# Performance work log

Measured on AMD Instinct MI355X. Metric: run time of the kernel, lower is better.

The kernel has to match this reference:

```python
import jax, jax.numpy as jnp
import numpy as np

B, T, CM, CZ, H = 2, 512, 256, 128, 16
DH = CM // H  # 16
EPS = 1e-5


def setup_inputs() -> dict:
    root = jax.random.key(0)
    ks = jax.random.split(root, 16)
    n = lambda i, shape: jax.random.normal(ks[i], shape, dtype=jnp.float32)
    s = np.float32(1.0 / np.sqrt(CM))
    return dict(
        query=n(0, (B, T, CM)),
        key=n(1, (B, T, CM)),
        value=n(2, (B, T, CM)),
        pos_embedding=n(3, (B, 2 * T - 1, CM)),  # T2 = 2T-1 relative positions
        z=n(4, (B, T, T, CZ)),
        mask=jax.random.randint(ks[5], (B, 1, T), 0, 2) > 0,
        Wq=n(6, (CM, CM)) * s, bq=jnp.zeros((CM,), jnp.float32),
        Wk=n(7, (CM, CM)) * s, bk=jnp.zeros((CM,), jnp.float32),
        Wv=n(8, (CM, CM)) * s, bv=jnp.zeros((CM,), jnp.float32),
        Wp=n(9, (CM, CM)) * s,
        u_bias=n(10, (H, DH)) * np.float32(0.1),
        v_bias=n(11, (H, DH)) * np.float32(0.1),
        Wo=n(12, (CM, CM)) * s, bo=jnp.zeros((CM,), jnp.float32),
        ln_g=jnp.ones((CZ,), jnp.float32), ln_b=jnp.zeros((CZ,), jnp.float32),
        Wz=n(13, (CZ, H)) * np.float32(1.0 / np.sqrt(CZ)),
    )


def _relative_shift(ps):
    # ps: (B, H, T1, T2) -> Transformer-XL relative shift, keep first T2//2+1 cols
    b, h, t1, t2 = ps.shape
    padded = jnp.pad(ps, ((0, 0), (0, 0), (0, 0), (1, 0)))  # (b,h,t1,t2+1)
    padded = padded.reshape(b, h, t2 + 1, t1)
    shifted = padded[:, :, 1:, :].reshape(b, h, t1, t2)
    return shifted[..., : t2 // 2 + 1]


def reference(query, key, value, pos_embedding, z, mask,
              Wq, bq, Wk, bk, Wv, bv, Wp, u_bias, v_bias, Wo, bo,
              ln_g, ln_b, Wz):
    b = query.shape[0]
    q = (query @ Wq.T + bq).reshape(b, -1, H, DH)          # (b,T,H,dh)
    k = (key @ Wk.T + bk).reshape(b, -1, H, DH)
    v = (value @ Wv.T + bv).reshape(b, -1, H, DH)
    p = (pos_embedding @ Wp.T).reshape(b, -1, H, DH)       # (b,2T-1,H,dh)

    content = jnp.einsum('bihd,bjhd->bhij', q + u_bias, k)     # (b,H,T,T)
    pos = jnp.einsum('bihd,bjhd->bhij', q + v_bias, p)         # (b,H,T,2T-1)
    pos = _relative_shift(pos)                                  # (b,H,T,T)

    # z bias: LayerNorm over c_z then project to heads (chunking in torch is a no-op math-wise)
    mu = jnp.mean(z, axis=-1, keepdims=True)
    var = jnp.var(z, axis=-1, keepdims=True)
    zn = (z - mu) * jax.lax.rsqrt(var + EPS) * ln_g + ln_b
    z_bias = jnp.einsum('bijc,ch->bhij', zn, Wz)                # (b,H,T,T)

    score = (content + pos) / np.float32(np.sqrt(DH)) + z_bias
    score = jnp.where(mask[:, None, :, :], jnp.float32(-10000.0), score)
    attn = jax.nn.softmax(score, axis=-1)  # dropout is identity in eval

    ctx = jnp.einsum('bhij,bjhd->bihd', attn, v).reshape(b, -1, CM)
    return ctx @ Wo.T + bo
```

## Files before the change

### kernel.cpp

```cpp
#include <hip/hip_runtime.h>
#include <hip/hip_bf16.h>

typedef __attribute__((ext_vector_type(8))) short short8;
typedef __attribute__((ext_vector_type(4))) short short4v;
typedef __attribute__((ext_vector_type(4))) float f32x4;

#define LD4(dst, v4) { dst[0]=(v4).x; dst[1]=(v4).y; dst[2]=(v4).z; dst[3]=(v4).w; }

static __device__ __forceinline__ short f2bf(float f) {
    union { float f; unsigned u; } v; v.f = f;
    unsigned r = (v.u + 0x7FFFu + ((v.u >> 16) & 1u)) >> 16;
    return (short)r;
}
static __device__ __forceinline__ float bf2f(short s) {
    union { unsigned u; float f; } v; v.u = ((unsigned)(unsigned short)s) << 16;
    return v.f;
}

static __device__ __forceinline__ void proj_tile(
    const float* __restrict__ X, const float* __restrict__ W,
    const float* __restrict__ bias, float* __restrict__ Yf,
    short* __restrict__ Yb, int M, int base, float* xs)
{
    int rt = base >> 1, ct = base & 1;
    int t = threadIdx.x;
    int row_base = rt * 32;
    {
        int r = t >> 3, k0 = (t & 7) * 32;
        int row = row_base + r;
        if (row < M) {
            const float* xp = X + (size_t)row * 256 + k0;
            #pragma unroll
            for (int q = 0; q < 8; ++q) {
                float4 v = *(const float4*)(xp + q * 4);
                xs[(k0 + q * 4 + 0) * 36 + r] = v.x;
                xs[(k0 + q * 4 + 1) * 36 + r] = v.y;
                xs[(k0 + q * 4 + 2) * 36 + r] = v.z;
                xs[(k0 + q * 4 + 3) * 36 + r] = v.w;
            }
        } else {
            #pragma unroll
            for (int q = 0; q < 32; ++q) xs[(k0 + q) * 36 + r] = 0.f;
        }
    }
    __syncthreads();
    int c_base = ct * 128 + (t & 31) * 4;
    int r_base = (t >> 5) * 4;
    float acc[4][4];
    #pragma unroll
    for (int a = 0; a < 4; ++a)
        #pragma unroll
        for (int b = 0; b < 4; ++b) acc[a][b] = 0.f;
    for (int k = 0; k < 256; k += 4) {
        float w0[4], w1[4], w2[4], w3[4];
        { float4 v = *(const float4*)(W + (size_t)(c_base + 0) * 256 + k); LD4(w0, v); }
        { float4 v = *(const float4*)(W + (size_t)(c_base + 1) * 256 + k); LD4(w1, v); }
        { float4 v = *(const float4*)(W + (size_t)(c_base + 2) * 256 + k); LD4(w2, v); }
        { float4 v = *(const float4*)(W + (size_t)(c_base + 3) * 256 + k); LD4(w3, v); }
        #pragma unroll
        for (int kk = 0; kk < 4; ++kk) {
            float xl[4];
            float4 xv = *(const float4*)(&xs[(k + kk) * 36 + r_base]);
            LD4(xl, xv);
            #pragma unroll
            for (int ri = 0; ri < 4; ++ri) {
                acc[ri][0] += xl[ri] * w0[kk];
                acc[ri][1] += xl[ri] * w1[kk];
                acc[ri][2] += xl[ri] * w2[kk];
                acc[ri][3] += xl[ri] * w3[kk];
            }
        }
    }
    #pragma unroll
    for (int ri = 0; ri < 4; ++ri) {
        int row = row_base + r_base + ri;
        if (row < M) {
            float o0 = acc[ri][0] + (bias ? bias[c_base + 0] : 0.f);
            float o1 = acc[ri][1] + (bias ? bias[c_base + 1] : 0.f);
            float o2 = acc[ri][2] + (bias ? bias[c_base + 2] : 0.f);
            float o3 = acc[ri][3] + (bias ? bias[c_base + 3] : 0.f);
            if (Yb) {
                short4v o; o[0] = f2bf(o0); o[1] = f2bf(o1); o[2] = f2bf(o2); o[3] = f2bf(o3);
                *(short4v*)(Yb + (size_t)row * 256 + c_base) = o;
            } else {
                float4 o; o.x = o0; o.y = o1; o.z = o2; o.w = o3;
                *(float4*)(Yf + (size_t)row * 256 + c_base) = o;
            }
        }
    }
}

__global__ void k_proj(const float* __restrict__ query, const float* __restrict__ key,
                       const float* __restrict__ value, const float* __restrict__ pos,
                       const float* __restrict__ Wq, const float* __restrict__ bq,
                       const float* __restrict__ Wk, const float* __restrict__ bk,
                       const float* __restrict__ Wv, const float* __restrict__ bv,
                       const float* __restrict__ Wp,
                       const float* __restrict__ ln_g, const float* __restrict__ ln_b,
                       const float* __restrict__ Wz, const int* __restrict__ mask,
                       float* __restrict__ qb, short* __restrict__ kbf,
                       short* __restrict__ vbf, short* __restrict__ pbf,
                       short* __restrict__ wzp, float* __restrict__ Ch,
                       int* __restrict__ idx, int* __restrict__ cnt)
{
    __shared__ float xs[256 * 36];
    int bx = blockIdx.x;
    if (bx == 320) {
        int lane = threadIdx.x & 63, wave = threadIdx.x >> 6;
        if (wave == 0) {
            for (int b = 0; b < 2; ++b) {
                int* idxb = idx + b * 512;
                #pragma unroll
                for (int q = 0; q < 8; ++q) idxb[q * 64 + lane] = -1;
                int total = 0;
                for (int q = 0; q < 8; ++q) {
                    int j = q * 64 + lane;
                    int u = (mask[b * 512 + j] == 0) ? 1 : 0;
                    unsigned long long bal = __ballot(u);
                    int p = total + __popcll(bal & ((1ull << lane) - 1ull));
                    if (u) idxb[p] = j;
                    total += (int)__popcll(bal);
                }
                if (total == 0) {
                    for (int q = 0; q < 8; ++q) idxb[q * 64 + lane] = q * 64 + lane;
                    total = 512;
                }
                if (lane == 0) cnt[b] = total;
            }
        } else if (wave == 1) {
            for (int id = lane; id < 2048; id += 64) {
                int m = id >> 9, rem = id & 511, l = rem >> 3, ii = rem & 7;
                int c = m * 32 + ((l >> 4) << 3) + ii, h = l & 15;
                wzp[id] = f2bf(ln_g[c] * Wz[c * 16 + h]);
            }
        } else if (wave == 2) {
            if (lane < 16) {
                float cc = 0.f;
                for (int c = 0; c < 128; ++c) cc += ln_b[c] * Wz[c * 16 + lane];
                Ch[lane] = cc;
            }
        }
        return;
    }
    if (bx < 64)       proj_tile(query, Wq, bq, qb, nullptr, 1024, bx, xs);
    else if (bx < 128) proj_tile(key,   Wk, bk, nullptr, kbf, 1024, bx - 64, xs);
    else if (bx < 192) proj_tile(value, Wv, bv, nullptr, vbf, 1024, bx - 128, xs);
    else               proj_tile(pos,   Wp, nullptr, nullptr, pbf, 2046, bx - 192, xs);
}

__global__ void __launch_bounds__(256, 6) k_zc(
    const float* __restrict__ z, const short* __restrict__ wzp,
    const int* __restrict__ idx, const int* __restrict__ cnt,
    const short* __restrict__ kbf, const short* __restrict__ vbf,
    short* __restrict__ kbfC, short* __restrict__ vbTC,
    short* __restrict__ zacc, float* __restrict__ rsbuf)
{
    __shared__ short st[32 * 264];
    int bx = blockIdx.x;
    const short8 z8 = {0,0,0,0,0,0,0,0};
    if (bx < 32) {
        int b = bx >> 4, jn0 = (bx & 15) * 32;
        int t = threadIdx.x;
        int r = t >> 3, cc = (t & 7) * 32;
        int jn = jn0 + r;
        int jv = idx[b * 512 + jn];
        {
            short* dst = kbfC + ((size_t)b * 512 + jn) * 256 + cc;
            if (jv >= 0) {
                const short* src = kbf + ((size_t)b * 512 + jv) * 256 + cc;
                #pragma unroll
                for (int q = 0; q < 4; ++q) *(short8*)(dst + q * 8) = *(const short8*)(src + q * 8);
            } else {
                #pragma unroll
                for (int q = 0; q < 4; ++q) *(short8*)(dst + q * 8) = z8;
            }
        }
        {
            if (jv >= 0) {
                const short* src = vbf + ((size_t)b * 512 + jv) * 256 + cc;
                #pragma unroll
                for (int q = 0; q < 4; ++q) *(short8*)(&st[r * 264 + cc + q * 8]) = *(const short8*)(src + q * 8);
            } else {
                #pragma unroll
                for (int q = 0; q < 4; ++q) *(short8*)(&st[r * 264 + cc + q * 8]) = z8;
            }
            __syncthreads();
            int c = t;
            short tmp[32];
            #pragma unroll
            for (int q = 0; q < 32; ++q) tmp[q] = st[q * 264 + c];
            short* dst = vbTC + ((size_t)b * 256 + c) * 512 + jn0;
            #pragma unroll
            for (int q = 0; q < 4; ++q) *(short8*)(dst + q * 8) = *(const short8*)(&tmp[q * 8]);
        }
        return;
    }
    int wave = threadIdx.x >> 6, lane = threadIdx.x & 63;
    int w = (bx - 32) * 4 + wave;
    int bi = w >> 5, tl = w & 31;
    int b = bi >> 9;
    int np = (min(cnt[b], 512) + 31) & ~31;
    if (tl * 16 >= np) return;
    int h = lane & 15, g = lane >> 4;
    short8 wz[4];
    #pragma unroll
    for (int m = 0; m < 4; ++m) wz[m] = *(const short8*)(wzp + m * 512 + lane * 8);
    int jv = idx[b * 512 + tl * 16 + h];
    int jr = (jv < 0) ? 0 : jv;
    const float* zr = z + ((size_t)bi * 512 + jr) * 128 + g * 8;
    float4 xa[4], xb[4];
    #pragma unroll
    for (int m = 0; m < 4; ++m) {
        xa[m] = *(const float4*)(zr + m * 32);
        xb[m] = *(const float4*)(zr + m * 32 + 4);
    }
    float sum = 0.f, sq = 0.f;
    #pragma unroll
    for (int m = 0; m < 4; ++m) {
        sum += xa[m].x + xa[m].y + xa[m].z + xa[m].w + xb[m].x + xb[m].y + xb[m].z + xb[m].w;
        sq  += xa[m].x*xa[m].x + xa[m].y*xa[m].y + xa[m].z*xa[m].z + xa[m].w*xa[m].w
             + xb[m].x*xb[m].x + xb[m].y*xb[m].y + xb[m].z*xb[m].z + xb[m].w*xb[m].w;
    }
    sum += __shfl_xor(sum, 16); sum += __shfl_xor(sum, 32);
    sq  += __shfl_xor(sq, 16);  sq  += __shfl_xor(sq, 32);
    float mu = sum * (1.f / 128.f);
    float rs = rsqrtf(sq * (1.f / 128.f) - mu * mu + 1e-5f);
    f32x4 acc = {0.f, 0.f, 0.f, 0.f};
    #pragma unroll
    for (int m = 0; m < 4; ++m) {
        short8 af;
        af[0] = f2bf(xa[m].x - mu); af[1] = f2bf(xa[m].y - mu);
        af[2] = f2bf(xa[m].z - mu); af[3] = f2bf(xa[m].w - mu);
        af[4] = f2bf(xb[m].x - mu); af[5] = f2bf(xb[m].y - mu);
        af[6] = f2bf(xb[m].z - mu); af[7] = f2bf(xb[m].w - mu);
        acc = __builtin_amdgcn_mfma_f32_16x16x32_bf16(af, wz[m], acc, 0, 0, 0);
    }
    short4v o; o[0] = f2bf(acc[0]); o[1] = f2bf(acc[1]); o[2] = f2bf(acc[2]); o[3] = f2bf(acc[3]);
    *(short4v*)(zacc + ((size_t)bi * 16 + h) * 512 + tl * 16 + g * 4) = o;
    if (g == 0) rsbuf[(size_t)bi * 512 + tl * 16 + h] = rs;
}

__global__ void __launch_bounds__(256, 4) k_attn3(
    const float* __restrict__ qb, const short* __restrict__ kbfC, const short* __restrict__ pbf,
    const short* __restrict__ zacc, const float* __restrict__ rsbuf, const float* __restrict__ Ch,
    const float* __restrict__ u_bias, const float* __restrict__ v_bias,
    const int* __restrict__ idx, const int* __restrict__ cnt,
    const short* __restrict__ vbTC, float* __restrict__ ctx)
{
    __shared__ short wT[16 * 520];
    __shared__ float redm[64], reds[64];
    const short8 zero8 = {0, 0, 0, 0, 0, 0, 0, 0};

    int bi = blockIdx.x;
    int b = bi >> 9, i = bi & 511;
    int t = threadIdx.x;
    int lane = t & 63, wave = t >> 6;
    int h = lane & 15, g = lane >> 4;
    float ch = Ch[h];
    int np = (min(cnt[b], 512) + 31) & ~31;
    int nt16 = np >> 4;

    bool act = ((h & 1) == (g >> 1));
    int m_act = act ? (h >> 1) : 8;
    short8 qu8 = zero8, qv8 = zero8;
    {
        int c0q = h * 16 + (g & 1) * 8;
        const float* qp = qb + (size_t)bi * 256 + c0q;
        #pragma unroll
        for (int ii = 0; ii < 8; ++ii) {
            float qv_ = qp[ii];
            qu8[ii] = f2bf(0.25f * (qv_ + u_bias[c0q + ii]));
            qv8[ii] = f2bf(0.25f * (qv_ + v_bias[c0q + ii]));
        }
        if (!act) { qu8 = zero8; qv8 = zero8; }
    }

    f32x4 sc[8];
    float mloc = -3.0e38f;
    #pragma unroll
    for (int q = 0; q < 8; ++q) {
        int tl = wave + q * 4;
        if (tl < nt16) {
            int jn = tl * 16 + h;
            int jvh = idx[b * 512 + jn];
            int jrp = 511 + ((jvh < 0) ? 0 : jvh) - i;
            const short* kr = kbfC + ((size_t)b * 512 + jn) * 256 + g * 8;
            const short* pr = pbf + ((size_t)b * 1023 + jrp) * 256 + g * 8;
            f32x4 acp = {0.f, 0.f, 0.f, 0.f};
            #pragma unroll
            for (int m = 0; m < 8; ++m) {
                short8 ka = *(const short8*)(kr + m * 32);
                short8 pa = *(const short8*)(pr + m * 32);
                short8 bu = (m == m_act) ? qu8 : zero8;
                short8 bv = (m == m_act) ? qv8 : zero8;
                acp = __builtin_amdgcn_mfma_f32_16x16x32_bf16(ka, bu, acp, 0, 0, 0);
                acp = __builtin_amdgcn_mfma_f32_16x16x32_bf16(pa, bv, acp, 0, 0, 0);
            }
            short4v za = *(const short4v*)(zacc + ((size_t)bi * 16 + h) * 512 + tl * 16 + g * 4);
            float4 rs4 = *(const float4*)(rsbuf + (size_t)bi * 512 + tl * 16 + g * 4);
            int4 jv4 = *(const int4*)(idx + b * 512 + tl * 16 + g * 4);
            float rr[4]; LD4(rr, rs4);
            int jj4[4]; jj4[0] = jv4.x; jj4[1] = jv4.y; jj4[2] = jv4.z; jj4[3] = jv4.w;
            #pragma unroll
            for (int reg = 0; reg < 4; ++reg) {
                float s = acp[reg] + rr[reg] * bf2f(za[reg]) + ch;
                s = (jj4[reg] < 0) ? -3.0e38f : s;
                sc[q][reg] = s;
                mloc = fmaxf(mloc, s);
            }
        }
    }

    mloc = fmaxf(mloc, __shfl_xor(mloc, 16));
    mloc = fmaxf(mloc, __shfl_xor(mloc, 32));
    redm[wave * 16 + h] = mloc;
    __syncthreads();
    float mg = fmaxf(fmaxf(redm[h], redm[16 + h]), fmaxf(redm[32 + h], redm[48 + h]));
    float ssum = 0.f;
    #pragma unroll
    for (int q = 0; q < 8; ++q) {
        int tl = wave + q * 4;
        if (tl < nt16) {
            #pragma unroll
            for (int reg = 0; reg < 4; ++reg) {
                float e = __expf(sc[q][reg] - mg);
                sc[q][reg] = e;
                ssum += e;
            }
        }
    }
    ssum += __shfl_xor(ssum, 16); ssum += __shfl_xor(ssum, 32);
    reds[wave * 16 + h] = ssum;
    __syncthreads();
    float sg = reds[h] + reds[16 + h] + reds[32 + h] + reds[48 + h];
    float inv = 1.f / sg;
    #pragma unroll
    for (int q = 0; q < 8; ++q) {
        int tl = wave + q * 4;
        if (tl < nt16) {
            short4v w4;
            #pragma unroll
            for (int reg = 0; reg < 4; ++reg) w4[reg] = f2bf(sc[q][reg] * inv);
            *(short4v*)(&wT[h * 520 + tl * 16 + g * 4]) = w4;
        }
    }
    __syncthreads();

    #pragma unroll
    for (int q = 0; q < 4; ++q) {
        int hp = wave * 4 + q;
        int c0 = hp * 16;
        const short* vrow = vbTC + ((size_t)b * 256 + c0 + h) * 512;
        f32x4 a0 = {0.f, 0.f, 0.f, 0.f};
        for (int jn0 = 0; jn0 < np; jn0 += 32) {
            short8 wA = *(const short8*)(&wT[hp * 520 + jn0 + g * 8]);
            short8 vB = *(const short8*)(vrow + jn0 + g * 8);
            a0 = __builtin_amdgcn_mfma_f32_16x16x32_bf16(wA, vB, a0, 0, 0, 0);
        }
        if (g == 0) ctx[(size_t)bi * 256 + c0 + h] = a0[0];
    }
}

__global__ void proj_o(const float* __restrict__ X, const float* __restrict__ W,
                       const float* __restrict__ bias, float* __restrict__ Y)
{
    __shared__ float xs[256 * 36];
    proj_tile(X, W, bias, Y, nullptr, 1024, blockIdx.x, xs);
}

extern "C" void kernel_launch(void* const* d_in, const int* in_sizes, int n_in,
                              void* d_out, int out_size, void* d_ws, size_t ws_size,
                              hipStream_t stream) {
    const float* query = (const float*)d_in[0];
    const float* key   = (const float*)d_in[1];
    const float* value = (const float*)d_in[2];
    const float* pos   = (const float*)d_in[3];
    const float* z     = (const float*)d_in[4];
    const int*   mask  = (const int*)d_in[5];
    const float* Wq = (const float*)d_in[6];
    const float* bq = (const float*)d_in[7];
    const float* Wk = (const float*)d_in[8];
    const float* bk = (const float*)d_in[9];
    const float* Wv = (const float*)d_in[10];
    const float* bv = (const float*)d_in[11];
    const float* Wp = (const float*)d_in[12];
    const float* u_bias = (const float*)d_in[13];
    const float* v_bias = (const float*)d_in[14];
    const float* Wo = (const float*)d_in[15];
    const float* bo = (const float*)d_in[16];
    const float* ln_g = (const float*)d_in[17];
    const float* ln_b = (const float*)d_in[18];
    const float* Wz = (const float*)d_in[19];

    char* ws = (char*)d_ws;
    float* qb   = (float*)(ws + 0);
    short* kbf  = (short*)(ws + (1u << 20));
    short* vbf  = (short*)(ws + 1572864u);
    short* pbf  = (short*)(ws + (2u << 20));
    short* wzp  = (short*)(ws + (3u << 20));
    float* Ch   = (float*)(ws + (3u << 20) + 4096);
    int*   idx  = (int*)(ws + (3u << 20) + 8192);
    int*   cnt  = (int*)(ws + (3u << 20) + 16384);
    short* kbfC = (short*)(ws + (4u << 20));
    short* vbTC = (short*)(ws + 4718592u);
    short* zacc = (short*)(ws + (5u << 20));
    float* rsbuf= (float*)(ws + (22u << 20));
    float* ctx  = (float*)(ws + (24u << 20));

    hipLaunchKernelGGL(k_proj, dim3(321), dim3(256), 0, stream,
                       query, key, value, pos, Wq, bq, Wk, bk, Wv, bv, Wp,
                       ln_g, ln_b, Wz, mask,
                       qb, kbf, vbf, pbf, wzp, Ch, idx, cnt);
    hipLaunchKernelGGL(k_zc, dim3(8224), dim3(256), 0, stream,
                       z, wzp, idx, cnt, kbf, vbf, kbfC, vbTC, zacc, rsbuf);
    hipLaunchKernelGGL(k_attn3, dim3(1024), dim3(256), 0, stream,
                       qb, kbfC, pbf, zacc, rsbuf, Ch, u_bias, v_bias, idx, cnt, vbTC, ctx);
    hipLaunchKernelGGL(proj_o, dim3(64), dim3(256), 0, stream, ctx, Wo, bo, (float*)d_out);
}
```

Measured before the change: 191.2 us.

## Fold LayerNorm mean/scale into z-bias epilogue and halve projection tile rows

The z LayerNorm is refactored so raw z is converted to bf16 and fed to the MFMA directly. The mean and rstd are applied afterwards via a precomputed per-head sum of ln_g*Wz (Ah), and the final z-bias is finalised inside k_z. This removes the rsbuf buffer and its per-score load and FMA in the attention kernel, and shortens the z kernel's register lifetime. Projection tiles shrink from 32 to 16 rows, doubling block counts for k_proj and proj_o to improve occupancy on the many-CU GPU. The cost is more redundant W reads per block and some bf16 precision risk, since z is quantised before its mean is subtracted.

```diff
diff --git a/kernel.cpp b/kernel.cpp
--- a/kernel.cpp
+++ b/kernel.cpp
@@ -17,38 +17,38 @@
     return v.f;
 }
 
-static __device__ __forceinline__ void proj_tile(
+static __device__ __forceinline__ void proj_tile16(
     const float* __restrict__ X, const float* __restrict__ W,
     const float* __restrict__ bias, float* __restrict__ Yf,
     short* __restrict__ Yb, int M, int base, float* xs)
 {
     int rt = base >> 1, ct = base & 1;
     int t = threadIdx.x;
-    int row_base = rt * 32;
+    int row_base = rt * 16;
     {
-        int r = t >> 3, k0 = (t & 7) * 32;
+        int r = t & 15, kq = (t >> 4) * 16;
         int row = row_base + r;
         if (row < M) {
-            const float* xp = X + (size_t)row * 256 + k0;
-            #pragma unroll
-            for (int q = 0; q < 8; ++q) {
+            const float* xp = X + (size_t)row * 256 + kq;
+            #pragma unroll
+            for (int q = 0; q < 4; ++q) {
                 float4 v = *(const float4*)(xp + q * 4);
-                xs[(k0 + q * 4 + 0) * 36 + r] = v.x;
-                xs[(k0 + q * 4 + 1) * 36 + r] = v.y;
-                xs[(k0 + q * 4 + 2) * 36 + r] = v.z;
-                xs[(k0 + q * 4 + 3) * 36 + r] = v.w;
+                xs[(kq + q * 4 + 0) * 18 + r] = v.x;
+                xs[(kq + q * 4 + 1) * 18 + r] = v.y;
+                xs[(kq + q * 4 + 2) * 18 + r] = v.z;
+                xs[(kq + q * 4 + 3) * 18 + r] = v.w;
             }
         } else {
             #pragma unroll
-            for (int q = 0; q < 32; ++q) xs[(k0 + q) * 36 + r] = 0.f;
+            for (int q = 0; q < 16; ++q) xs[(kq + q) * 18 + r] = 0.f;
         }
     }
     __syncthreads();
     int c_base = ct * 128 + (t & 31) * 4;
-    int r_base = (t >> 5) * 4;
-    float acc[4][4];
-    #pragma unroll
-    for (int a = 0; a < 4; ++a)
+    int r_base = (t >> 5) * 2;
+    float acc[2][4];
+    #pragma unroll
+    for (int a = 0; a < 2; ++a)
         #pragma unroll
         for (int b = 0; b < 4; ++b) acc[a][b] = 0.f;
     for (int k = 0; k < 256; k += 4) {
@@ -59,20 +59,16 @@
         { float4 v = *(const float4*)(W + (size_t)(c_base + 3) * 256 + k); LD4(w3, v); }
         #pragma unroll
         for (int kk = 0; kk < 4; ++kk) {
-            float xl[4];
-            float4 xv = *(const float4*)(&xs[(k + kk) * 36 + r_base]);
-            LD4(xl, xv);
-            #pragma unroll
-            for (int ri = 0; ri < 4; ++ri) {
-                acc[ri][0] += xl[ri] * w0[kk];
-                acc[ri][1] += xl[ri] * w1[kk];
-                acc[ri][2] += xl[ri] * w2[kk];
-                acc[ri][3] += xl[ri] * w3[kk];
-            }
-        }
-    }
-    #pragma unroll
-    for (int ri = 0; ri < 4; ++ri) {
+            float x0 = xs[(k + kk) * 18 + r_base];
+            float x1 = xs[(k + kk) * 18 + r_base + 1];
+            acc[0][0] += x0 * w0[kk]; acc[0][1] += x0 * w1[kk];
+            acc[0][2] += x0 * w2[kk]; acc[0][3] += x0 * w3[kk];
+            acc[1][0] += x1 * w0[kk]; acc[1][1] += x1 * w1[kk];
+            acc[1][2] += x1 * w2[kk]; acc[1][3] += x1 * w3[kk];
+        }
+    }
+    #pragma unroll
+    for (int ri = 0; ri < 2; ++ri) {
         int row = row_base + r_base + ri;
         if (row < M) {
             float o0 = acc[ri][0] + (bias ? bias[c_base + 0] : 0.f);
@@ -90,22 +86,23 @@
     }
 }
 
-__global__ void k_proj(const float* __restrict__ query, const float* __restrict__ key,
-                       const float* __restrict__ value, const float* __restrict__ pos,
-                       const float* __restrict__ Wq, const float* __restrict__ bq,
-                       const float* __restrict__ Wk, const float* __restrict__ bk,
-                       const float* __restrict__ Wv, const float* __restrict__ bv,
-                       const float* __restrict__ Wp,
-                       const float* __restrict__ ln_g, const float* __restrict__ ln_b,
-                       const float* __restrict__ Wz, const int* __restrict__ mask,
-                       float* __restrict__ qb, short* __restrict__ kbf,
-                       short* __restrict__ vbf, short* __restrict__ pbf,
-                       short* __restrict__ wzp, float* __restrict__ Ch,
-                       int* __restrict__ idx, int* __restrict__ cnt)
+__global__ void __launch_bounds__(256, 4) k_proj(
+    const float* __restrict__ query, const float* __restrict__ key,
+    const float* __restrict__ value, const float* __restrict__ pos,
+    const float* __restrict__ Wq, const float* __restrict__ bq,
+    const float* __restrict__ Wk, const float* __restrict__ bk,
+    const float* __restrict__ Wv, const float* __restrict__ bv,
+    const float* __restrict__ Wp,
+    const float* __restrict__ ln_g, const float* __restrict__ ln_b,
+    const float* __restrict__ Wz, const int* __restrict__ mask,
+    float* __restrict__ qb, short* __restrict__ kbf,
+    short* __restrict__ vbf, short* __restrict__ pbf,
+    short* __restrict__ wzp, float* __restrict__ Ah, float* __restrict__ Ch,
+    int* __restrict__ idx, int* __restrict__ cnt)
 {
-    __shared__ float xs[256 * 36];
+    __shared__ float xs[256 * 18];
     int bx = blockIdx.x;
-    if (bx == 320) {
+    if (bx == 640) {
         int lane = threadIdx.x & 63, wave = threadIdx.x >> 6;
         if (wave == 0) {
             for (int b = 0; b < 2; ++b) {
@@ -134,26 +131,32 @@
                 wzp[id] = f2bf(ln_g[c] * Wz[c * 16 + h]);
             }
         } else if (wave == 2) {
-            if (lane < 16) {
-                float cc = 0.f;
-                for (int c = 0; c < 128; ++c) cc += ln_b[c] * Wz[c * 16 + lane];
-                Ch[lane] = cc;
-            }
+            int h = lane & 15, part = lane >> 4;
+            float a = 0.f, c = 0.f;
+            #pragma unroll 4
+            for (int cc = part * 32; cc < part * 32 + 32; ++cc) {
+                float wv = Wz[cc * 16 + h];
+                a += ln_g[cc] * wv;
+                c += ln_b[cc] * wv;
+            }
+            a += __shfl_xor(a, 16); a += __shfl_xor(a, 32);
+            c += __shfl_xor(c, 16); c += __shfl_xor(c, 32);
+            if (part == 0) { Ah[h] = a; Ch[h] = c; }
         }
         return;
     }
-    if (bx < 64)       proj_tile(query, Wq, bq, qb, nullptr, 1024, bx, xs);
-    else if (bx < 128) proj_tile(key,   Wk, bk, nullptr, kbf, 1024, bx - 64, xs);
-    else if (bx < 192) proj_tile(value, Wv, bv, nullptr, vbf, 1024, bx - 128, xs);
-    else               proj_tile(pos,   Wp, nullptr, nullptr, pbf, 2046, bx - 192, xs);
-}
-
-__global__ void __launch_bounds__(256, 6) k_zc(
+    if (bx < 128)      proj_tile16(query, Wq, bq, qb, nullptr, 1024, bx, xs);
+    else if (bx < 256) proj_tile16(key,   Wk, bk, nullptr, kbf, 1024, bx - 128, xs);
+    else if (bx < 384) proj_tile16(value, Wv, bv, nullptr, vbf, 1024, bx - 256, xs);
+    else               proj_tile16(pos,   Wp, nullptr, nullptr, pbf, 2046, bx - 384, xs);
+}
+
+__global__ void __launch_bounds__(256, 6) k_z(
     const float* __restrict__ z, const short* __restrict__ wzp,
+    const float* __restrict__ Ah, const float* __restrict__ Ch,
     const int* __restrict__ idx, const int* __restrict__ cnt,
     const short* __restrict__ kbf, const short* __restrict__ vbf,
-    short* __restrict__ kbfC, short* __restrict__ vbTC,
-    short* __restrict__ zacc, float* __restrict__ rsbuf)
+    short* __restrict__ kbfC, short* __restrict__ vbTC, short* __restrict__ zacc)
 {
     __shared__ short st[32 * 264];
     int bx = blockIdx.x;
@@ -208,18 +211,18 @@
     int jv = idx[b * 512 + tl * 16 + h];
     int jr = (jv < 0) ? 0 : jv;
     const float* zr = z + ((size_t)bi * 512 + jr) * 128 + g * 8;
-    float4 xa[4], xb[4];
+    float sum = 0.f, sq = 0.f;
+    short8 af[4];
     #pragma unroll
     for (int m = 0; m < 4; ++m) {
-        xa[m] = *(const float4*)(zr + m * 32);
-        xb[m] = *(const float4*)(zr + m * 32 + 4);
-    }
-    float sum = 0.f, sq = 0.f;
-    #pragma unroll
-    for (int m = 0; m < 4; ++m) {
-        sum += xa[m].x + xa[m].y + xa[m].z + xa[m].w + xb[m].x + xb[m].y + xb[m].z + xb[m].w;
-        sq  += xa[m].x*xa[m].x + xa[m].y*xa[m].y + xa[m].z*xa[m].z + xa[m].w*xa[m].w
-             + xb[m].x*xb[m].x + xb[m].y*xb[m].y + xb[m].z*xb[m].z + xb[m].w*xb[m].w;
+        float4 a = *(const float4*)(zr + m * 32);
+        float4 c = *(const float4*)(zr + m * 32 + 4);
+        sum += a.x + a.y + a.z + a.w + c.x + c.y + c.z + c.w;
+        sq  += a.x*a.x + a.y*a.y + a.z*a.z + a.w*a.w + c.x*c.x + c.y*c.y + c.z*c.z + c.w*c.w;
+        short8 s8;
+        s8[0] = f2bf(a.x); s8[1] = f2bf(a.y); s8[2] = f2bf(a.z); s8[3] = f2bf(a.w);
+        s8[4] = f2bf(c.x); s8[5] = f2bf(c.y); s8[6] = f2bf(c.z); s8[7] = f2bf(c.w);
+        af[m] = s8;
     }
     sum += __shfl_xor(sum, 16); sum += __shfl_xor(sum, 32);
     sq  += __shfl_xor(sq, 16);  sq  += __shfl_xor(sq, 32);
@@ -227,22 +230,23 @@
     float rs = rsqrtf(sq * (1.f / 128.f) - mu * mu + 1e-5f);
     f32x4 acc = {0.f, 0.f, 0.f, 0.f};
     #pragma unroll
-    for (int m = 0; m < 4; ++m) {
-        short8 af;
-        af[0] = f2bf(xa[m].x - mu); af[1] = f2bf(xa[m].y - mu);
-        af[2] = f2bf(xa[m].z - mu); af[3] = f2bf(xa[m].w - mu);
-        af[4] = f2bf(xb[m].x - mu); af[5] = f2bf(xb[m].y - mu);
-        af[6] = f2bf(xb[m].z - mu); af[7] = f2bf(xb[m].w - mu);
-        acc = __builtin_amdgcn_mfma_f32_16x16x32_bf16(af, wz[m], acc, 0, 0, 0);
-    }
-    short4v o; o[0] = f2bf(acc[0]); o[1] = f2bf(acc[1]); o[2] = f2bf(acc[2]); o[3] = f2bf(acc[3]);
+    for (int m = 0; m < 4; ++m)
+        acc = __builtin_amdgcn_mfma_f32_16x16x32_bf16(af[m], wz[m], acc, 0, 0, 0);
+    float ah = Ah[h], ch = Ch[h];
+    short4v o;
+    #pragma unroll
+    for (int reg = 0; reg < 4; ++reg) {
+        int orow = g * 4 + reg;
+        float mo = __shfl(mu, orow);
+        float ro = __shfl(rs, orow);
+        o[reg] = f2bf(ro * (acc[reg] - mo * ah) + ch);
+    }
     *(short4v*)(zacc + ((size_t)bi * 16 + h) * 512 + tl * 16 + g * 4) = o;
-    if (g == 0) rsbuf[(size_t)bi * 512 + tl * 16 + h] = rs;
 }
 
 __global__ void __launch_bounds__(256, 4) k_attn3(
     const float* __restrict__ qb, const short* __restrict__ kbfC, const short* __restrict__ pbf,
-    const short* __restrict__ zacc, const float* __restrict__ rsbuf, const float* __restrict__ Ch,
+    const short* __restrict__ zacc,
     const float* __restrict__ u_bias, const float* __restrict__ v_bias,
     const int* __restrict__ idx, const int* __restrict__ cnt,
     const short* __restrict__ vbTC, float* __restrict__ ctx)
@@ -256,7 +260,6 @@
     int t = threadIdx.x;
     int lane = t & 63, wave = t >> 6;
     int h = lane & 15, g = lane >> 4;
-    float ch = Ch[h];
     int np = (min(cnt[b], 512) + 31) & ~31;
     int nt16 = np >> 4;
 
@@ -297,13 +300,11 @@
                 acp = __builtin_amdgcn_mfma_f32_16x16x32_bf16(pa, bv, acp, 0, 0, 0);
             }
             short4v za = *(const short4v*)(zacc + ((size_t)bi * 16 + h) * 512 + tl * 16 + g * 4);
-            float4 rs4 = *(const float4*)(rsbuf + (size_t)bi * 512 + tl * 16 + g * 4);
             int4 jv4 = *(const int4*)(idx + b * 512 + tl * 16 + g * 4);
-            float rr[4]; LD4(rr, rs4);
             int jj4[4]; jj4[0] = jv4.x; jj4[1] = jv4.y; jj4[2] = jv4.z; jj4[3] = jv4.w;
             #pragma unroll
             for (int reg = 0; reg < 4; ++reg) {
-                float s = acp[reg] + rr[reg] * bf2f(za[reg]) + ch;
+                float s = acp[reg] + bf2f(za[reg]);
                 s = (jj4[reg] < 0) ? -3.0e38f : s;
                 sc[q][reg] = s;
                 mloc = fmaxf(mloc, s);
@@ -361,11 +362,12 @@
     }
 }
 
-__global__ void proj_o(const float* __restrict__ X, const float* __restrict__ W,
-                       const float* __restrict__ bias, float* __restrict__ Y)
+__global__ void __launch_bounds__(256, 4) proj_o(
+    const float* __restrict__ X, const float* __restrict__ W,
+    const float* __restrict__ bias, float* __restrict__ Y)
 {
-    __shared__ float xs[256 * 36];
-    proj_tile(X, W, bias, Y, nullptr, 1024, blockIdx.x, xs);
+    __shared__ float xs[256 * 18];
+    proj_tile16(X, W, bias, Y, nullptr, 1024, blockIdx.x, xs);
 }
 
 extern "C" void kernel_launch(void* const* d_in, const int* in_sizes, int n_in,
@@ -398,22 +400,22 @@
     short* vbf  = (short*)(ws + 1572864u);
     short* pbf  = (short*)(ws + (2u << 20));
     short* wzp  = (short*)(ws + (3u << 20));
-    float* Ch   = (float*)(ws + (3u << 20) + 4096);
+    float* Ah   = (float*)(ws + (3u << 20) + 4096);
+    float* Ch   = (float*)(ws + (3u << 20) + 4160);
     int*   idx  = (int*)(ws + (3u << 20) + 8192);
     int*   cnt  = (int*)(ws + (3u << 20) + 16384);
     short* kbfC = (short*)(ws + (4u << 20));
     short* vbTC = (short*)(ws + 4718592u);
     short* zacc = (short*)(ws + (5u << 20));
-    float* rsbuf= (float*)(ws + (22u << 20));
-    float* ctx  = (float*)(ws + (24u << 20));
-
-    hipLaunchKernelGGL(k_proj, dim3(321), dim3(256), 0, stream,
+    float* ctx  = (float*)(ws + (22u << 20));
+
+    hipLaunchKernelGGL(k_proj, dim3(641), dim3(256), 0, stream,
                        query, key, value, pos, Wq, bq, Wk, bk, Wv, bv, Wp,
                        ln_g, ln_b, Wz, mask,
-                       qb, kbf, vbf, pbf, wzp, Ch, idx, cnt);
-    hipLaunchKernelGGL(k_zc, dim3(8224), dim3(256), 0, stream,
-                       z, wzp, idx, cnt, kbf, vbf, kbfC, vbTC, zacc, rsbuf);
+                       qb, kbf, vbf, pbf, wzp, Ah, Ch, idx, cnt);
+    hipLaunchKernelGGL(k_z, dim3(8224), dim3(256), 0, stream,
+                       z, wzp, Ah, Ch, idx, cnt, kbf, vbf, kbfC, vbTC, zacc);
     hipLaunchKernelGGL(k_attn3, dim3(1024), dim3(256), 0, stream,
-                       qb, kbfC, pbf, zacc, rsbuf, Ch, u_bias, v_bias, idx, cnt, vbTC, ctx);
-    hipLaunchKernelGGL(proj_o, dim3(64), dim3(256), 0, stream, ctx, Wo, bo, (float*)d_out);
-}
+                       qb, kbfC, pbf, zacc, u_bias, v_bias, idx, cnt, vbTC, ctx);
+    hipLaunchKernelGGL(proj_o, dim3(128), dim3(256), 0, stream, ctx, Wo, bo, (float*)d_out);
+}
```

Result: slower. 214.5 us (+12.1%).

## Fold LayerNorm affine into z-bias, stage z via LDS, fuse output projection

Applied to the files above, without the earlier changes.

The z LayerNorm is now applied algebraically after the Wz projection (rs*(acc - mu*A_h) + C_h), so the finished z-bias is written once and the separate rsbuf array and its reads in attention are dropped. z rows are gathered through LDS with coalesced float4 loads and packed to bf16 using v_cvt_pk_bf16_f32. The output projection with Wo is fused into the tail of the attention kernel, which removes the ctx round trip and one launch. The cost is a per-block 256x256 GEMV that rereads Wo in every one of the 1024 blocks, lower z precision because statistics are now computed from bf16-rounded values, and a lower occupancy hint on k_z.

```diff
diff --git a/kernel.cpp b/kernel.cpp
--- a/kernel.cpp
+++ b/kernel.cpp
@@ -15,6 +15,11 @@
 static __device__ __forceinline__ float bf2f(short s) {
     union { unsigned u; float f; } v; v.u = ((unsigned)(unsigned short)s) << 16;
     return v.f;
+}
+static __device__ __forceinline__ unsigned cvt_pk_bf16(float lo, float hi) {
+    unsigned r;
+    asm volatile("v_cvt_pk_bf16_f32 %0, %1, %2" : "=v"(r) : "v"(lo), "v"(hi));
+    return r;
 }
 
 static __device__ __forceinline__ void proj_tile(
@@ -100,7 +105,7 @@
                        const float* __restrict__ Wz, const int* __restrict__ mask,
                        float* __restrict__ qb, short* __restrict__ kbf,
                        short* __restrict__ vbf, short* __restrict__ pbf,
-                       short* __restrict__ wzp, float* __restrict__ Ch,
+                       short* __restrict__ wzp, float* __restrict__ Ah, float* __restrict__ Ch,
                        int* __restrict__ idx, int* __restrict__ cnt)
 {
     __shared__ float xs[256 * 36];
@@ -134,11 +139,17 @@
                 wzp[id] = f2bf(ln_g[c] * Wz[c * 16 + h]);
             }
         } else if (wave == 2) {
-            if (lane < 16) {
-                float cc = 0.f;
-                for (int c = 0; c < 128; ++c) cc += ln_b[c] * Wz[c * 16 + lane];
-                Ch[lane] = cc;
-            }
+            int h = lane & 15, part = lane >> 4;
+            float a = 0.f, c = 0.f;
+            #pragma unroll 4
+            for (int cc = part * 32; cc < part * 32 + 32; ++cc) {
+                float wv = Wz[cc * 16 + h];
+                a += ln_g[cc] * wv;
+                c += ln_b[cc] * wv;
+            }
+            a += __shfl_xor(a, 16); a += __shfl_xor(a, 32);
+            c += __shfl_xor(c, 16); c += __shfl_xor(c, 32);
+            if (part == 0) { Ah[h] = a; Ch[h] = c; }
         }
         return;
     }
@@ -148,17 +159,18 @@
     else               proj_tile(pos,   Wp, nullptr, nullptr, pbf, 2046, bx - 192, xs);
 }
 
-__global__ void __launch_bounds__(256, 6) k_zc(
+__global__ void __launch_bounds__(256, 4) k_z(
     const float* __restrict__ z, const short* __restrict__ wzp,
+    const float* __restrict__ Ah, const float* __restrict__ Ch,
     const int* __restrict__ idx, const int* __restrict__ cnt,
     const short* __restrict__ kbf, const short* __restrict__ vbf,
-    short* __restrict__ kbfC, short* __restrict__ vbTC,
-    short* __restrict__ zacc, float* __restrict__ rsbuf)
+    short* __restrict__ kbfC, short* __restrict__ vbTC, short* __restrict__ zacc)
 {
-    __shared__ short st[32 * 264];
+    __shared__ short ldsb[8448];
     int bx = blockIdx.x;
-    const short8 z8 = {0,0,0,0,0,0,0,0};
+    const short8 z8v = {0,0,0,0,0,0,0,0};
     if (bx < 32) {
+        short* st = ldsb;
         int b = bx >> 4, jn0 = (bx & 15) * 32;
         int t = threadIdx.x;
         int r = t >> 3, cc = (t & 7) * 32;
@@ -172,7 +184,7 @@
                 for (int q = 0; q < 4; ++q) *(short8*)(dst + q * 8) = *(const short8*)(src + q * 8);
             } else {
                 #pragma unroll
-                for (int q = 0; q < 4; ++q) *(short8*)(dst + q * 8) = z8;
+                for (int q = 0; q < 4; ++q) *(short8*)(dst + q * 8) = z8v;
             }
         }
         {
@@ -182,7 +194,7 @@
                 for (int q = 0; q < 4; ++q) *(short8*)(&st[r * 264 + cc + q * 8]) = *(const short8*)(src + q * 8);
             } else {
                 #pragma unroll
-                for (int q = 0; q < 4; ++q) *(short8*)(&st[r * 264 + cc + q * 8]) = z8;
+                for (int q = 0; q < 4; ++q) *(short8*)(&st[r * 264 + cc + q * 8]) = z8v;
             }
             __syncthreads();
             int c = t;
@@ -201,25 +213,42 @@
     int b = bi >> 9;
     int np = (min(cnt[b], 512) + 31) & ~31;
     if (tl * 16 >= np) return;
+    short* zs = ldsb + wave * 2112;
+    const int* idxr = idx + b * 512 + tl * 16;
+    const float* zb_ = z + (size_t)bi * 65536;
+    int l5 = lane >> 5, l31 = lane & 31;
+    int idxv = idxr[lane & 15];
+    #pragma unroll
+    for (int m = 0; m < 8; ++m) {
+        int r = 2 * m + l5;
+        int jv = __shfl(idxv, r);
+        int jr = (jv < 0) ? 0 : jv;
+        float4 v = *(const float4*)(zb_ + (size_t)jr * 128 + l31 * 4);
+        uint2 pk;
+        pk.x = cvt_pk_bf16(v.x, v.y);
+        pk.y = cvt_pk_bf16(v.z, v.w);
+        *(uint2*)(&zs[r * 132 + l31 * 4]) = pk;
+    }
     int h = lane & 15, g = lane >> 4;
     short8 wz[4];
     #pragma unroll
     for (int m = 0; m < 4; ++m) wz[m] = *(const short8*)(wzp + m * 512 + lane * 8);
-    int jv = idx[b * 512 + tl * 16 + h];
-    int jr = (jv < 0) ? 0 : jv;
-    const float* zr = z + ((size_t)bi * 512 + jr) * 128 + g * 8;
-    float4 xa[4], xb[4];
+    short8 af[4];
+    float sum = 0.f, sq = 0.f;
     #pragma unroll
     for (int m = 0; m < 4; ++m) {
-        xa[m] = *(const float4*)(zr + m * 32);
-        xb[m] = *(const float4*)(zr + m * 32 + 4);
-    }
-    float sum = 0.f, sq = 0.f;
-    #pragma unroll
-    for (int m = 0; m < 4; ++m) {
-        sum += xa[m].x + xa[m].y + xa[m].z + xa[m].w + xb[m].x + xb[m].y + xb[m].z + xb[m].w;
-        sq  += xa[m].x*xa[m].x + xa[m].y*xa[m].y + xa[m].z*xa[m].z + xa[m].w*xa[m].w
-             + xb[m].x*xb[m].x + xb[m].y*xb[m].y + xb[m].z*xb[m].z + xb[m].w*xb[m].w;
+        short4v a0 = *(const short4v*)(&zs[h * 132 + g * 8 + m * 32]);
+        short4v a1 = *(const short4v*)(&zs[h * 132 + g * 8 + m * 32 + 4]);
+        short8 s8;
+        s8[0] = a0[0]; s8[1] = a0[1]; s8[2] = a0[2]; s8[3] = a0[3];
+        s8[4] = a1[0]; s8[5] = a1[1]; s8[6] = a1[2]; s8[7] = a1[3];
+        af[m] = s8;
+        #pragma unroll
+        for (int ii = 0; ii < 8; ++ii) {
+            float x = bf2f(s8[ii]);
+            sum += x;
+            sq = fmaf(x, x, sq);
+        }
     }
     sum += __shfl_xor(sum, 16); sum += __shfl_xor(sum, 32);
     sq  += __shfl_xor(sq, 16);  sq  += __shfl_xor(sq, 32);
@@ -227,28 +256,31 @@
     float rs = rsqrtf(sq * (1.f / 128.f) - mu * mu + 1e-5f);
     f32x4 acc = {0.f, 0.f, 0.f, 0.f};
     #pragma unroll
-    for (int m = 0; m < 4; ++m) {
-        short8 af;
-        af[0] = f2bf(xa[m].x - mu); af[1] = f2bf(xa[m].y - mu);
-        af[2] = f2bf(xa[m].z - mu); af[3] = f2bf(xa[m].w - mu);
-        af[4] = f2bf(xb[m].x - mu); af[5] = f2bf(xb[m].y - mu);
-        af[6] = f2bf(xb[m].z - mu); af[7] = f2bf(xb[m].w - mu);
-        acc = __builtin_amdgcn_mfma_f32_16x16x32_bf16(af, wz[m], acc, 0, 0, 0);
-    }
-    short4v o; o[0] = f2bf(acc[0]); o[1] = f2bf(acc[1]); o[2] = f2bf(acc[2]); o[3] = f2bf(acc[3]);
+    for (int m = 0; m < 4; ++m)
+        acc = __builtin_amdgcn_mfma_f32_16x16x32_bf16(af[m], wz[m], acc, 0, 0, 0);
+    float ah = Ah[h], ch = Ch[h];
+    short4v o;
+    #pragma unroll
+    for (int reg = 0; reg < 4; ++reg) {
+        int orow = g * 4 + reg;
+        float mo = __shfl(mu, orow);
+        float ro = __shfl(rs, orow);
+        o[reg] = f2bf(ro * (acc[reg] - mo * ah) + ch);
+    }
     *(short4v*)(zacc + ((size_t)bi * 16 + h) * 512 + tl * 16 + g * 4) = o;
-    if (g == 0) rsbuf[(size_t)bi * 512 + tl * 16 + h] = rs;
-}
-
-__global__ void __launch_bounds__(256, 4) k_attn3(
+}
+
+__global__ void __launch_bounds__(256, 4) k_attn4(
     const float* __restrict__ qb, const short* __restrict__ kbfC, const short* __restrict__ pbf,
-    const short* __restrict__ zacc, const float* __restrict__ rsbuf, const float* __restrict__ Ch,
+    const short* __restrict__ zacc,
     const float* __restrict__ u_bias, const float* __restrict__ v_bias,
     const int* __restrict__ idx, const int* __restrict__ cnt,
-    const short* __restrict__ vbTC, float* __restrict__ ctx)
+    const short* __restrict__ vbTC,
+    const float* __restrict__ Wo, const float* __restrict__ bo, float* __restrict__ out)
 {
     __shared__ short wT[16 * 520];
     __shared__ float redm[64], reds[64];
+    __shared__ float ctx_lds[256];
     const short8 zero8 = {0, 0, 0, 0, 0, 0, 0, 0};
 
     int bi = blockIdx.x;
@@ -256,7 +288,6 @@
     int t = threadIdx.x;
     int lane = t & 63, wave = t >> 6;
     int h = lane & 15, g = lane >> 4;
-    float ch = Ch[h];
     int np = (min(cnt[b], 512) + 31) & ~31;
     int nt16 = np >> 4;
 
@@ -297,13 +328,11 @@
                 acp = __builtin_amdgcn_mfma_f32_16x16x32_bf16(pa, bv, acp, 0, 0, 0);
             }
             short4v za = *(const short4v*)(zacc + ((size_t)bi * 16 + h) * 512 + tl * 16 + g * 4);
-            float4 rs4 = *(const float4*)(rsbuf + (size_t)bi * 512 + tl * 16 + g * 4);
             int4 jv4 = *(const int4*)(idx + b * 512 + tl * 16 + g * 4);
-            float rr[4]; LD4(rr, rs4);
             int jj4[4]; jj4[0] = jv4.x; jj4[1] = jv4.y; jj4[2] = jv4.z; jj4[3] = jv4.w;
             #pragma unroll
             for (int reg = 0; reg < 4; ++reg) {
-                float s = acp[reg] + rr[reg] * bf2f(za[reg]) + ch;
+                float s = acp[reg] + bf2f(za[reg]);
                 s = (jj4[reg] < 0) ? -3.0e38f : s;
                 sc[q][reg] = s;
                 mloc = fmaxf(mloc, s);
@@ -357,15 +386,24 @@
             short8 vB = *(const short8*)(vrow + jn0 + g * 8);
             a0 = __builtin_amdgcn_mfma_f32_16x16x32_bf16(wA, vB, a0, 0, 0, 0);
         }
-        if (g == 0) ctx[(size_t)bi * 256 + c0 + h] = a0[0];
-    }
-}
-
-__global__ void proj_o(const float* __restrict__ X, const float* __restrict__ W,
-                       const float* __restrict__ bias, float* __restrict__ Y)
-{
-    __shared__ float xs[256 * 36];
-    proj_tile(X, W, bias, Y, nullptr, 1024, blockIdx.x, xs);
+        if (g == 0) ctx_lds[c0 + h] = a0[0];
+    }
+    __syncthreads();
+
+    {
+        float acc = bo[t];
+        const float* wrow = Wo + (size_t)t * 256;
+        #pragma unroll 4
+        for (int k = 0; k < 256; k += 8) {
+            float4 w0 = *(const float4*)(wrow + k);
+            float4 w1 = *(const float4*)(wrow + k + 4);
+            acc += ctx_lds[k + 0] * w0.x + ctx_lds[k + 1] * w0.y
+                 + ctx_lds[k + 2] * w0.z + ctx_lds[k + 3] * w0.w
+                 + ctx_lds[k + 4] * w1.x + ctx_lds[k + 5] * w1.y
+                 + ctx_lds[k + 6] * w1.z + ctx_lds[k + 7] * w1.w;
+        }
+        out[(size_t)bi * 256 + t] = acc;
+    }
 }
 
 extern "C" void kernel_launch(void* const* d_in, const int* in_sizes, int n_in,
@@ -398,22 +436,21 @@
     short* vbf  = (short*)(ws + 1572864u);
     short* pbf  = (short*)(ws + (2u << 20));
     short* wzp  = (short*)(ws + (3u << 20));
-    float* Ch   = (float*)(ws + (3u << 20) + 4096);
+    float* Ah   = (float*)(ws + (3u << 20) + 4096);
+    float* Ch   = (float*)(ws + (3u << 20) + 4160);
     int*   idx  = (int*)(ws + (3u << 20) + 8192);
     int*   cnt  = (int*)(ws + (3u << 20) + 16384);
     short* kbfC = (short*)(ws + (4u << 20));
     short* vbTC = (short*)(ws + 4718592u);
     short* zacc = (short*)(ws + (5u << 20));
-    float* rsbuf= (float*)(ws + (22u << 20));
-    float* ctx  = (float*)(ws + (24u << 20));
 
     hipLaunchKernelGGL(k_proj, dim3(321), dim3(256), 0, stream,
                        query, key, value, pos, Wq, bq, Wk, bk, Wv, bv, Wp,
                        ln_g, ln_b, Wz, mask,
-                       qb, kbf, vbf, pbf, wzp, Ch, idx, cnt);
-    hipLaunchKernelGGL(k_zc, dim3(8224), dim3(256), 0, stream,
-                       z, wzp, idx, cnt, kbf, vbf, kbfC, vbTC, zacc, rsbuf);
-    hipLaunchKernelGGL(k_attn3, dim3(1024), dim3(256), 0, stream,
-                       qb, kbfC, pbf, zacc, rsbuf, Ch, u_bias, v_bias, idx, cnt, vbTC, ctx);
-    hipLaunchKernelGGL(proj_o, dim3(64), dim3(256), 0, stream, ctx, Wo, bo, (float*)d_out);
-}
+                       qb, kbf, vbf, pbf, wzp, Ah, Ch, idx, cnt);
+    hipLaunchKernelGGL(k_z, dim3(8224), dim3(256), 0, stream,
+                       z, wzp, Ah, Ch, idx, cnt, kbf, vbf, kbfC, vbTC, zacc);
+    hipLaunchKernelGGL(k_attn4, dim3(1024), dim3(256), 0, stream,
+                       qb, kbfC, pbf, zacc, u_bias, v_bias, idx, cnt, vbTC,
+                       Wo, bo, (float*)d_out);
+}
```

Result: faster. 183.9 us (-3.8%).
